# Kernel optimization log

Hardware: AMD Instinct MI355X
Metric: run time of the kernel (lower is better)

Reference implementation:

```python
import jax, jax.numpy as jnp
import numpy as np

B, C, L = 16384, 10000, 20


def setup_inputs() -> dict:
    key = jax.random.key(0)
    k1, k2 = jax.random.split(key)
    logits = jax.random.normal(k1, (B, C), dtype=jnp.float32)
    labels = jax.random.randint(k2, (B, L), 0, C, dtype=jnp.int64)
    return {"logits": logits, "labels": labels}


def reference(logits, labels):
    # Original: for each sample, for each tag until the first -1,
    # loss += F.cross_entropy(logits[idx], tag)  (sum over all valid tags).
    # Vectorized: one log-softmax pass + masked gather + sum.
    logp = jax.nn.log_softmax(logits, axis=-1)  # [B, C]
    # 'break' at first -1 -> prefix-validity mask along the label dim
    nonneg = (labels >= 0).astype(jnp.int32)
    valid = jnp.cumprod(nonneg, axis=1).astype(logp.dtype)  # [B, L]
    safe = jnp.where(valid > 0, labels, 0)  # in-range indices for gather
    gathered = jnp.take_along_axis(logp, safe, axis=1)  # [B, L]
    loss = -jnp.sum(gathered * valid)
    return loss
```

## Files before the change

### kernel.cpp

```cpp
#include <hip/hip_runtime.h>

constexpr int B = 16384;
constexpr int C = 10000;
constexpr int L = 20;
constexpr int THREADS = 256;
constexpr int VECS = C / 4;
constexpr int FULL_ITERS = VECS / THREADS;
constexpr int TAIL = VECS - FULL_ITERS * THREADS;

typedef float vfloat4 __attribute__((ext_vector_type(4)));

__global__ __launch_bounds__(THREADS) void row_loss_kernel(
    const float* __restrict__ logits,
    const int* __restrict__ labels,
    float* __restrict__ row_loss) {
  const int b = blockIdx.x;
  const int t = threadIdx.x;
  const int lane = t & 63;
  const int wid = t >> 6;

  const float* __restrict__ rowp = logits + (size_t)b * C;
  const vfloat4* __restrict__ row = reinterpret_cast<const vfloat4*>(rowp);

  int lab = 0;
  float g = 0.0f;
  if (wid == 0 && lane < L) {
    lab = labels[b * L + lane];
    int safe = (lab >= 0) ? lab : 0;
    g = rowp[safe];
  }

  float s0 = 0.0f, s1 = 0.0f, s2 = 0.0f, s3 = 0.0f;
  #pragma unroll
  for (int k = 0; k < FULL_ITERS; ++k) {
    vfloat4 v = row[t + k * THREADS];
    s0 += __expf(v.x);
    s1 += __expf(v.y);
    s2 += __expf(v.z);
    s3 += __expf(v.w);
  }
  if (t < TAIL) {
    vfloat4 v = row[FULL_ITERS * THREADS + t];
    s0 += __expf(v.x);
    s1 += __expf(v.y);
    s2 += __expf(v.z);
    s3 += __expf(v.w);
  }
  float s = (s0 + s1) + (s2 + s3);

  #pragma unroll
  for (int off = 32; off; off >>= 1) s += __shfl_xor(s, off);
  __shared__ float warp_s[THREADS / 64];
  if (lane == 0) warp_s[wid] = s;
  __syncthreads();
  const float lse = __logf(warp_s[0] + warp_s[1] + warp_s[2] + warp_s[3]);

  if (wid == 0) {
    unsigned long long mask = __ballot((lane < L) && (lab >= 0));
    float term = 0.0f;
    if (lane < L) {
      unsigned long long need = (1ull << (lane + 1)) - 1ull;
      if ((mask & need) == need) term = lse - g;
    }
    #pragma unroll
    for (int off = 32; off; off >>= 1) term += __shfl_xor(term, off);
    if (lane == 0) row_loss[b] = term;
  }
}

__global__ __launch_bounds__(256) void reduce_kernel(
    const float* __restrict__ row_loss, float* __restrict__ out) {
  const int t = threadIdx.x;
  float s = 0.0f;
  #pragma unroll 4
  for (int i = t; i < B; i += 256) s += row_loss[i];
  #pragma unroll
  for (int off = 32; off; off >>= 1) s += __shfl_xor(s, off);
  __shared__ float warp_s[4];
  const int lane = t & 63, wid = t >> 6;
  if (lane == 0) warp_s[wid] = s;
  __syncthreads();
  if (t == 0) out[0] = warp_s[0] + warp_s[1] + warp_s[2] + warp_s[3];
}

extern "C" void kernel_launch(void* const* d_in, const int* in_sizes, int n_in,
                              void* d_out, int out_size, void* d_ws, size_t ws_size,
                              hipStream_t stream) {
  const float* logits = (const float*)d_in[0];
  const int* labels = (const int*)d_in[1];
  float* row_loss = (float*)d_ws;
  float* out = (float*)d_out;

  row_loss_kernel<<<B, THREADS, 0, stream>>>(logits, labels, row_loss);
  reduce_kernel<<<1, 256, 0, stream>>>(row_loss, out);
}
```

Before: 810.9 us.

## Assign rows to single wavefronts with persistent grid instead of block-per-row

Replaces the one-block-per-row mapping with one 64-lane wavefront per row. A fixed grid of 2048 blocks loops over two rows per wave. This removes the shared-memory reduction and __syncthreads per row and cuts block launch overhead. In exchange, each wave handles a whole 10000-element row serially with fewer concurrent loads per row, and the fixed grid may leave less memory-level parallelism in flight.

```diff
diff --git a/kernel.cpp b/kernel.cpp
--- a/kernel.cpp
+++ b/kernel.cpp
@@ -4,9 +4,12 @@
 constexpr int C = 10000;
 constexpr int L = 20;
 constexpr int THREADS = 256;
+constexpr int BLOCKS = 2048;
+constexpr int WAVES = BLOCKS * (THREADS / 64);
+constexpr int ROWS_PER_WAVE = B / WAVES;
 constexpr int VECS = C / 4;
-constexpr int FULL_ITERS = VECS / THREADS;
-constexpr int TAIL = VECS - FULL_ITERS * THREADS;
+constexpr int WLOADS = VECS / 64;
+constexpr int WTAIL = VECS - WLOADS * 64;
 
 typedef float vfloat4 __attribute__((ext_vector_type(4)));
 
@@ -14,48 +17,45 @@
     const float* __restrict__ logits,
     const int* __restrict__ labels,
     float* __restrict__ row_loss) {
-  const int b = blockIdx.x;
-  const int t = threadIdx.x;
-  const int lane = t & 63;
-  const int wid = t >> 6;
-
-  const float* __restrict__ rowp = logits + (size_t)b * C;
-  const vfloat4* __restrict__ row = reinterpret_cast<const vfloat4*>(rowp);
-
-  int lab = 0;
-  float g = 0.0f;
-  if (wid == 0 && lane < L) {
-    lab = labels[b * L + lane];
-    int safe = (lab >= 0) ? lab : 0;
-    g = rowp[safe];
-  }
-
-  float s0 = 0.0f, s1 = 0.0f, s2 = 0.0f, s3 = 0.0f;
-  #pragma unroll
-  for (int k = 0; k < FULL_ITERS; ++k) {
-    vfloat4 v = row[t + k * THREADS];
-    s0 += __expf(v.x);
-    s1 += __expf(v.y);
-    s2 += __expf(v.z);
-    s3 += __expf(v.w);
-  }
-  if (t < TAIL) {
-    vfloat4 v = row[FULL_ITERS * THREADS + t];
-    s0 += __expf(v.x);
-    s1 += __expf(v.y);
-    s2 += __expf(v.z);
-    s3 += __expf(v.w);
-  }
-  float s = (s0 + s1) + (s2 + s3);
+  const int lane = threadIdx.x & 63;
+  const int gw = blockIdx.x * (THREADS >> 6) + (threadIdx.x >> 6);
 
   #pragma unroll
-  for (int off = 32; off; off >>= 1) s += __shfl_xor(s, off);
-  __shared__ float warp_s[THREADS / 64];
-  if (lane == 0) warp_s[wid] = s;
-  __syncthreads();
-  const float lse = __logf(warp_s[0] + warp_s[1] + warp_s[2] + warp_s[3]);
+  for (int rr = 0; rr < ROWS_PER_WAVE; ++rr) {
+    const int b = gw * ROWS_PER_WAVE + rr;
+    const float* __restrict__ rowp = logits + (size_t)b * C;
+    const vfloat4* __restrict__ row = reinterpret_cast<const vfloat4*>(rowp);
 
-  if (wid == 0) {
+    int lab = 0;
+    float g = 0.0f;
+    if (lane < L) {
+      lab = labels[b * L + lane];
+      int safe = (lab >= 0) ? lab : 0;
+      g = rowp[safe];
+    }
+
+    float s0 = 0.0f, s1 = 0.0f, s2 = 0.0f, s3 = 0.0f;
+    #pragma unroll 13
+    for (int j = 0; j < WLOADS; ++j) {
+      vfloat4 v = row[lane + j * 64];
+      s0 += __expf(v.x);
+      s1 += __expf(v.y);
+      s2 += __expf(v.z);
+      s3 += __expf(v.w);
+    }
+    if (lane < WTAIL) {
+      vfloat4 v = row[WLOADS * 64 + lane];
+      s0 += __expf(v.x);
+      s1 += __expf(v.y);
+      s2 += __expf(v.z);
+      s3 += __expf(v.w);
+    }
+    float s = (s0 + s1) + (s2 + s3);
+
+    #pragma unroll
+    for (int off = 32; off; off >>= 1) s += __shfl_xor(s, off);
+    const float lse = __logf(s);
+
     unsigned long long mask = __ballot((lane < L) && (lab >= 0));
     float term = 0.0f;
     if (lane < L) {
@@ -91,6 +91,6 @@
   float* row_loss = (float*)d_ws;
   float* out = (float*)d_out;
 
-  row_loss_kernel<<<B, THREADS, 0, stream>>>(logits, labels, row_loss);
+  row_loss_kernel<<<BLOCKS, THREADS, 0, stream>>>(logits, labels, row_loss);
   reduce_kernel<<<1, 256, 0, stream>>>(row_loss, out);
 }
```

New measurement: 818.1 us. No clear change (+0.9%).
